# Performance work log

Measured on AMD Instinct MI355X. Metric: run time of the kernel, lower is better.

Reference implementation:

```python
import jax, jax.numpy as jnp
import numpy as np

P, B, FEAT, HID, ATTN, NHEAD = 4096, 32, 512, 512, 512, 8
HD = ATTN // NHEAD  # 64


def setup_inputs() -> dict:
    key = jax.random.key(0)
    ks = jax.random.split(key, 12)
    s = lambda n: 1.0 / np.sqrt(n)
    return {
        "last_hidden": jax.random.normal(ks[0], (1, B, HID), jnp.float32),
        "encoder_outputs": jax.random.normal(ks[1], (P, B, FEAT), jnp.float32),
        # outer projections (stored [in, out]; torch Linear is x @ W.T + b)
        "Wa_w": jax.random.uniform(ks[2], (FEAT, ATTN), jnp.float32, -s(FEAT), s(FEAT)),
        "Wa_b": jax.random.uniform(ks[3], (ATTN,), jnp.float32, -s(FEAT), s(FEAT)),
        "Ua_w": jax.random.uniform(ks[4], (HID, ATTN), jnp.float32, -s(HID), s(HID)),
        "Ua_b": jax.random.uniform(ks[5], (ATTN,), jnp.float32, -s(HID), s(HID)),
        # inner Attention(head_attn_size, head_attn_size, head_attn_size)
        "Wa2_w": jax.random.uniform(ks[6], (HD, HD), jnp.float32, -s(HD), s(HD)),
        "Wa2_b": jax.random.uniform(ks[7], (HD,), jnp.float32, -s(HD), s(HD)),
        "Ua2_w": jax.random.uniform(ks[8], (HD, HD), jnp.float32, -s(HD), s(HD)),
        "Ua2_b": jax.random.uniform(ks[9], (HD,), jnp.float32, -s(HD), s(HD)),
        "va_w": jax.random.uniform(ks[10], (HD, 1), jnp.float32, -s(HD), s(HD)),
        "va_b": jax.random.uniform(ks[11], (1,), jnp.float32, -s(HD), s(HD)),
        "nhead": NHEAD,
    }


def reference(last_hidden, encoder_outputs, Wa_w, Wa_b, Ua_w, Ua_b,
              Wa2_w, Wa2_b, Ua2_w, Ua2_b, va_w, va_b, nhead):
    p, b = encoder_outputs.shape[:2]
    enc = encoder_outputs @ Wa_w + Wa_b            # [P,B,A]
    hid = last_hidden @ Ua_w + Ua_b                # [1,B,A]
    hd = enc.shape[-1] // nhead
    enc = enc.reshape(p, b, nhead, hd)             # [P,B,nh,hd]
    hid = hid.reshape(1, b, nhead, hd)             # [1,B,nh,hd]
    # inner Bahdanau attention
    a = jnp.tanh((enc @ Wa2_w + Wa2_b) + (hid @ Ua2_w + Ua2_b))
    scores = a @ va_w + va_b                       # [P,B,nh,1]
    weights = jax.nn.softmax(scores, axis=0)       # softmax over pixels
    context = jnp.sum(weights * enc, axis=0, keepdims=True)  # [1,B,nh,hd]
    weight = jnp.mean(weights, axis=-2)            # mean over heads -> [P,B,1]
    context = context.reshape(1, b, nhead * hd)    # [1,B,A]
    return context, weight
```

## Files before the change

### kernel.cpp

```cpp
#include <hip/hip_runtime.h>
#include <hip/hip_bf16.h>

#define PDIM 4096
#define BDIM 32
#define MDIM (PDIM*BDIM)
#define KDIM 512
#define NDIM 512
#define NH   8
#define HD   64

typedef __attribute__((ext_vector_type(4))) float f32x4;
typedef __attribute__((ext_vector_type(8))) short bf16x8;

__device__ __forceinline__ unsigned short f2bf(float f) {
  unsigned u = __float_as_uint(f);
  u += 0x7fffu + ((u >> 16) & 1u);
  return (unsigned short)(u >> 16);
}
__device__ __forceinline__ float bf2f(unsigned short u) {
  return __uint_as_float(((unsigned)u) << 16);
}

__device__ __forceinline__ float fast_tanh(float x) {
  x = fminf(fmaxf(x, -15.f), 15.f);
  float e = __expf(2.f * x);
  return __fdividef(e - 1.f, e + 1.f);
}

#define GLOAD_LDS16(g, l) __builtin_amdgcn_global_load_lds( \
    (const __attribute__((address_space(1))) void*)(g),     \
    (__attribute__((address_space(3))) void*)(l), 16, 0, 0)

__global__ __launch_bounds__(256) void cvt_k(
    const float* __restrict__ x, unsigned short* __restrict__ xbf) {
  size_t i = ((size_t)blockIdx.x * 256 + threadIdx.x) * 8;
  float4 a = *(const float4*)(x + i);
  float4 b = *(const float4*)(x + i + 4);
  ushort4 o0; o0.x = f2bf(a.x); o0.y = f2bf(a.y); o0.z = f2bf(a.z); o0.w = f2bf(a.w);
  ushort4 o1; o1.x = f2bf(b.x); o1.y = f2bf(b.y); o1.z = f2bf(b.z); o1.w = f2bf(b.w);
  *(ushort4*)(xbf + i) = o0;
  *(ushort4*)(xbf + i + 4) = o1;
}

__global__ __launch_bounds__(512) void hub_k(
    const float* __restrict__ lh, const float* __restrict__ Ua,
    const float* __restrict__ Ua_b, const float* __restrict__ Ua2,
    const float* __restrict__ Ua2_b, const float* __restrict__ Wa_b,
    const float* __restrict__ Wa2, const float* __restrict__ Wa2_b,
    float* __restrict__ ubf) {
  int b = blockIdx.x, tid = threadIdx.x;
  __shared__ float ls[512];
  __shared__ float hs[512];
  ls[tid] = lh[b*512 + tid];
  __syncthreads();
  float s = Ua_b[tid];
  #pragma unroll 8
  for (int k = 0; k < 512; ++k)
    s += ls[k] * Ua[(size_t)k*512 + tid];
  hs[tid] = s;
  __syncthreads();
  int h = tid >> 6, j = tid & 63;
  float u = Ua2_b[j] + Wa2_b[j];
  #pragma unroll 4
  for (int k = 0; k < 64; ++k) {
    u += hs[h*64 + k] * Ua2[k*64 + j];
    u += Wa_b[h*64 + k] * Wa2[k*64 + j];
  }
  ubf[b*512 + tid] = u;
}

__global__ __launch_bounds__(256) void wft_k(
    const float* __restrict__ Wa, const float* __restrict__ Wa2,
    unsigned short* __restrict__ WfT) {
  int n = blockIdx.x, tid = threadIdx.x;
  int h = n >> 6, j = n & 63;
  __shared__ float w2[64];
  if (tid < 64) w2[tid] = Wa2[tid*64 + j];
  __syncthreads();
  for (int k = tid; k < 512; k += 256) {
    float s = 0.f;
    #pragma unroll 8
    for (int kk = 0; kk < 64; ++kk)
      s += Wa[(size_t)k*512 + h*64 + kk] * w2[kk];
    WfT[(size_t)n*512 + k] = f2bf(s);
  }
}

__global__ __launch_bounds__(256, 3) void gemm_score_k(
    const unsigned short* __restrict__ xbf, const unsigned short* __restrict__ WfT,
    const float* __restrict__ ubf, const float* __restrict__ va_w,
    const float* __restrict__ va_b, float* __restrict__ scores) {
  __shared__ __align__(16) unsigned short As[8192];
  __shared__ __align__(16) unsigned short Bs[8192];
  __shared__ float ubf_s[32*128];
  int tid = threadIdx.x;
  int bn = blockIdx.x, bm = blockIdx.y;
  int m0 = bm*128, n0 = bn*128;
  #pragma unroll
  for (int t = 0; t < 16; ++t) {
    int idx = t*256 + tid;
    ubf_s[idx] = ubf[(idx >> 7)*512 + n0 + (idx & 127)];
  }
  int lane = tid & 63, w = tid >> 6;
  int quad = lane >> 4, l16 = lane & 15;
  int wr = w >> 1, wc = w & 1;
  f32x4 acc[4][4] = {};

  for (int k0 = 0; k0 < KDIM; k0 += 64) {
    __syncthreads();
    #pragma unroll
    for (int i = 0; i < 4; ++i) {
      int c = i*256 + tid;
      int r = c & 127, kc = c >> 7;
      GLOAD_LDS16(xbf + (size_t)(m0 + r)*512 + k0 + kc*8, As + (size_t)c*8);
    }
    #pragma unroll
    for (int i = 0; i < 4; ++i) {
      int c = i*256 + tid;
      int r = c & 127, kc = c >> 7;
      GLOAD_LDS16(WfT + (size_t)(n0 + r)*512 + k0 + kc*8, Bs + (size_t)c*8);
    }
    __syncthreads();
    #pragma unroll
    for (int kk = 0; kk < 64; kk += 32) {
      int kc = (kk >> 3) + quad;
      bf16x8 af[4], bfr[4];
      #pragma unroll
      for (int ti = 0; ti < 4; ++ti)
        af[ti] = *(const bf16x8*)(As + ((size_t)kc*128 + 64*wr + 16*ti + l16)*8);
      #pragma unroll
      for (int tj = 0; tj < 4; ++tj)
        bfr[tj] = *(const bf16x8*)(Bs + ((size_t)kc*128 + 64*wc + 16*tj + l16)*8);
      #pragma unroll
      for (int ti = 0; ti < 4; ++ti)
        #pragma unroll
        for (int tj = 0; tj < 4; ++tj)
          acc[ti][tj] = __builtin_amdgcn_mfma_f32_16x16x32_bf16(
              af[ti], bfr[tj], acc[ti][tj], 0, 0, 0);
    }
  }

  int head = bn*2 + wc;
  float va_r[4];
  #pragma unroll
  for (int tj = 0; tj < 4; ++tj) va_r[tj] = va_w[16*tj + l16];
  float vb = va_b[0];
  #pragma unroll
  for (int ti = 0; ti < 4; ++ti) {
    #pragma unroll
    for (int r = 0; r < 4; ++r) {
      int row_loc = 64*wr + 16*ti + 4*quad + r;
      int b31 = row_loc & 31;
      float s = 0.f;
      #pragma unroll
      for (int tj = 0; tj < 4; ++tj) {
        float xa = acc[ti][tj][r] + ubf_s[b31*128 + 64*wc + 16*tj + l16];
        s += fast_tanh(xa) * va_r[tj];
      }
      s += __shfl_xor(s, 1); s += __shfl_xor(s, 2);
      s += __shfl_xor(s, 4); s += __shfl_xor(s, 8);
      if (l16 == 0) scores[(size_t)(m0 + row_loc)*NH + head] = s + vb;
    }
  }
}

__global__ __launch_bounds__(256) void softmax_k(
    const float* __restrict__ sc, float* __restrict__ w) {
  int b = blockIdx.x >> 3, h = blockIdx.x & 7;
  int tid = threadIdx.x;
  float v[16];
  float mx = -1e30f;
  #pragma unroll
  for (int i = 0; i < 16; ++i) {
    int p = tid + i*256;
    v[i] = sc[(size_t)(p*32 + b)*NH + h];
    mx = fmaxf(mx, v[i]);
  }
  for (int m = 1; m < 64; m <<= 1) mx = fmaxf(mx, __shfl_xor(mx, m));
  __shared__ float redm[4], reds[4];
  int wid = tid >> 6, lane = tid & 63;
  if (lane == 0) redm[wid] = mx;
  __syncthreads();
  mx = fmaxf(fmaxf(redm[0], redm[1]), fmaxf(redm[2], redm[3]));
  float sum = 0.f;
  #pragma unroll
  for (int i = 0; i < 16; ++i) { v[i] = __expf(v[i] - mx); sum += v[i]; }
  for (int m = 1; m < 64; m <<= 1) sum += __shfl_xor(sum, m);
  if (lane == 0) reds[wid] = sum;
  __syncthreads();
  sum = reds[0] + reds[1] + reds[2] + reds[3];
  float inv = 1.f / sum;
  #pragma unroll
  for (int i = 0; i < 16; ++i) {
    int p = tid + i*256;
    w[(size_t)(p*32 + b)*NH + h] = v[i] * inv;
  }
}

__global__ __launch_bounds__(256) void mean_k(
    const float* __restrict__ w, float* __restrict__ out) {
  int m = blockIdx.x*256 + threadIdx.x;
  const float4* p = (const float4*)(w + (size_t)m*NH);
  float4 a = p[0], c = p[1];
  out[BDIM*NDIM + m] = (a.x+a.y+a.z+a.w + c.x+c.y+c.z+c.w) * 0.125f;
}

__global__ __launch_bounds__(256) void ctx_partial_k(
    const unsigned short* __restrict__ xbf, const float* __restrict__ w,
    float* __restrict__ part) {
  int pc = blockIdx.x;
  int b  = blockIdx.y;
  int tid = threadIdx.x;
  __shared__ float wl[256*8];
  __shared__ float red[4][512];
  {
    const float4* wp = (const float4*)(w + ((size_t)((pc*256 + tid)*32 + b))*NH);
    float4 a = wp[0], c = wp[1];
    float4* dst = (float4*)(wl + tid*8);
    dst[0] = a; dst[1] = c;
  }
  __syncthreads();
  int lane = tid & 63, wv = tid >> 6;
  float acc[8][8];
  #pragma unroll
  for (int h = 0; h < 8; ++h)
    #pragma unroll
    for (int j = 0; j < 8; ++j) acc[h][j] = 0.f;
  for (int i = 0; i < 64; ++i) {
    int pl = wv*64 + i;
    bf16x8 xv = *(const bf16x8*)(xbf + ((size_t)((pc*256 + pl)*32 + b))*512 + lane*8);
    float xf[8];
    #pragma unroll
    for (int j = 0; j < 8; ++j) xf[j] = bf2f((unsigned short)xv[j]);
    #pragma unroll
    for (int h = 0; h < 8; ++h) {
      float ww = wl[pl*8 + h];
      #pragma unroll
      for (int j = 0; j < 8; ++j) acc[h][j] += ww * xf[j];
    }
  }
  for (int h = 0; h < 8; ++h) {
    #pragma unroll
    for (int j = 0; j < 8; j += 4)
      *(float4*)(&red[wv][lane*8 + j]) = *(float4*)(&acc[h][j]);
    __syncthreads();
    if (tid < 64) {
      #pragma unroll
      for (int j = 0; j < 8; ++j) {
        int f = tid*8 + j;
        part[((size_t)(b*16 + pc)*NH + h)*512 + f] =
            red[0][f] + red[1][f] + red[2][f] + red[3][f];
      }
    }
    __syncthreads();
  }
}

__global__ __launch_bounds__(256) void ctx_reduce_k(
    const float* __restrict__ part, float* __restrict__ cx) {
  int gid = blockIdx.x*256 + threadIdx.x;
  int f = gid & 511;
  int bh = gid >> 9;
  int h = bh & 7, b = bh >> 3;
  float s = 0.f;
  #pragma unroll
  for (int pc = 0; pc < 16; ++pc)
    s += part[((size_t)(b*16 + pc)*NH + h)*512 + f];
  cx[gid] = s;
}

__global__ __launch_bounds__(256) void ctx_proj_k(
    const float* __restrict__ cx, const float* __restrict__ Wa,
    const float* __restrict__ Wa_b, float* __restrict__ out) {
  int b = blockIdx.x >> 3, h = blockIdx.x & 7;
  int tid = threadIdx.x;
  __shared__ float cs[512];
  cs[tid]       = cx[(size_t)blockIdx.x*512 + tid];
  cs[tid + 256] = cx[(size_t)blockIdx.x*512 + tid + 256];
  __syncthreads();
  int d = tid & 63, g = tid >> 6;
  float s = 0.f;
  #pragma unroll 8
  for (int f = g*128; f < g*128 + 128; ++f)
    s += cs[f] * Wa[(size_t)f*512 + h*64 + d];
  __shared__ float red[256];
  red[tid] = s;
  __syncthreads();
  if (tid < 64) {
    float tot = red[tid] + red[64+tid] + red[128+tid] + red[192+tid] + Wa_b[h*64 + tid];
    out[b*512 + h*64 + tid] = tot;
  }
}

extern "C" void kernel_launch(void* const* d_in, const int* in_sizes, int n_in,
                              void* d_out, int out_size, void* d_ws, size_t ws_size,
                              hipStream_t stream) {
  (void)in_sizes; (void)n_in; (void)out_size; (void)ws_size;
  const float* lh    = (const float*)d_in[0];
  const float* x     = (const float*)d_in[1];
  const float* Wa_w  = (const float*)d_in[2];
  const float* Wa_b  = (const float*)d_in[3];
  const float* Ua_w  = (const float*)d_in[4];
  const float* Ua_b  = (const float*)d_in[5];
  const float* Wa2_w = (const float*)d_in[6];
  const float* Wa2_b = (const float*)d_in[7];
  const float* Ua2_w = (const float*)d_in[8];
  const float* Ua2_b = (const float*)d_in[9];
  const float* va_w  = (const float*)d_in[10];
  const float* va_b  = (const float*)d_in[11];
  float* out = (float*)d_out;
  char* ws = (char*)d_ws;

  unsigned short* xbf = (unsigned short*)(ws);
  unsigned short* WfT = (unsigned short*)(ws + 134217728);
  float* ubf    = (float*)(ws + 134742016);
  float* scores = (float*)(ws + 134807552);
  float* w      = (float*)(ws + 139001856);
  float* part   = (float*)(ws + 143196160);
  float* cx     = (float*)(ws + 151584768);

  hipLaunchKernelGGL(cvt_k, dim3(32768), dim3(256), 0, stream, x, xbf);
  hipLaunchKernelGGL(hub_k, dim3(32), dim3(512), 0, stream,
                     lh, Ua_w, Ua_b, Ua2_w, Ua2_b, Wa_b, Wa2_w, Wa2_b, ubf);
  hipLaunchKernelGGL(wft_k, dim3(512), dim3(256), 0, stream, Wa_w, Wa2_w, WfT);
  hipLaunchKernelGGL(gemm_score_k, dim3(4, 1024), dim3(256), 0, stream,
                     xbf, WfT, ubf, va_w, va_b, scores);
  hipLaunchKernelGGL(softmax_k, dim3(256), dim3(256), 0, stream, scores, w);
  hipLaunchKernelGGL(mean_k, dim3(512), dim3(256), 0, stream, w, out);
  hipLaunchKernelGGL(ctx_partial_k, dim3(16, 32), dim3(256), 0, stream, xbf, w, part);
  hipLaunchKernelGGL(ctx_reduce_k, dim3(512), dim3(256), 0, stream, part, cx);
  hipLaunchKernelGGL(ctx_proj_k, dim3(256), dim3(256), 0, stream, cx, Wa_w, Wa_b, out);
}
```

Baseline: 658.8 us.

## Double-buffer GEMM tiles, remap blocks, and transpose scores for coalesced softmax

The score GEMM now double-buffers its A/B LDS tiles so the next K-slice's global-to-LDS loads are issued before the current slice's MFMAs. It also uses a 1D grid with a block-index remap across groups of eight. The ubf tile is loaded into the reused A buffer after the main loop, with row padding to reduce LDS bank conflicts. Scores and weights are stored in a [head][batch][pixel] layout so softmax, mean and the context partial kernel read contiguous float4 or coalesced data instead of stride-8 accesses. The trade-offs are lower occupancy (launch bounds drop from 3 to 2), and mean_k now runs on only 16 blocks, each thread summing 256 values.

```diff
diff --git a/kernel.cpp b/kernel.cpp
--- a/kernel.cpp
+++ b/kernel.cpp
@@ -86,51 +86,66 @@
   }
 }
 
-__global__ __launch_bounds__(256, 3) void gemm_score_k(
+__global__ __launch_bounds__(256, 2) void gemm_score_k(
     const unsigned short* __restrict__ xbf, const unsigned short* __restrict__ WfT,
     const float* __restrict__ ubf, const float* __restrict__ va_w,
     const float* __restrict__ va_b, float* __restrict__ scores) {
-  __shared__ __align__(16) unsigned short As[8192];
-  __shared__ __align__(16) unsigned short Bs[8192];
-  __shared__ float ubf_s[32*128];
-  int tid = threadIdx.x;
-  int bn = blockIdx.x, bm = blockIdx.y;
+  __shared__ __align__(16) unsigned short As[2][8192];
+  __shared__ __align__(16) unsigned short Bs[2][8192];
+  int tid = threadIdx.x;
+  int orig = blockIdx.x;
+  int wg = (orig & 7) * 512 + (orig >> 3);
+  int bn = wg & 3, bm = wg >> 2;
   int m0 = bm*128, n0 = bn*128;
-  #pragma unroll
-  for (int t = 0; t < 16; ++t) {
-    int idx = t*256 + tid;
-    ubf_s[idx] = ubf[(idx >> 7)*512 + n0 + (idx & 127)];
-  }
   int lane = tid & 63, w = tid >> 6;
   int quad = lane >> 4, l16 = lane & 15;
   int wr = w >> 1, wc = w & 1;
   f32x4 acc[4][4] = {};
 
-  for (int k0 = 0; k0 < KDIM; k0 += 64) {
-    __syncthreads();
-    #pragma unroll
-    for (int i = 0; i < 4; ++i) {
-      int c = i*256 + tid;
-      int r = c & 127, kc = c >> 7;
-      GLOAD_LDS16(xbf + (size_t)(m0 + r)*512 + k0 + kc*8, As + (size_t)c*8);
-    }
-    #pragma unroll
-    for (int i = 0; i < 4; ++i) {
-      int c = i*256 + tid;
-      int r = c & 127, kc = c >> 7;
-      GLOAD_LDS16(WfT + (size_t)(n0 + r)*512 + k0 + kc*8, Bs + (size_t)c*8);
-    }
-    __syncthreads();
+  #pragma unroll
+  for (int i = 0; i < 4; ++i) {
+    int c = i*256 + tid;
+    int r = c & 127, kc = c >> 7;
+    GLOAD_LDS16(xbf + (size_t)(m0 + r)*512 + kc*8, &As[0][(size_t)c*8]);
+  }
+  #pragma unroll
+  for (int i = 0; i < 4; ++i) {
+    int c = i*256 + tid;
+    int r = c & 127, kc = c >> 7;
+    GLOAD_LDS16(WfT + (size_t)(n0 + r)*512 + kc*8, &Bs[0][(size_t)c*8]);
+  }
+  __syncthreads();
+
+  #pragma unroll
+  for (int t = 0; t < 8; ++t) {
+    int cur = t & 1, nxt = cur ^ 1;
+    if (t < 7) {
+      int kn = (t + 1) * 64;
+      #pragma unroll
+      for (int i = 0; i < 4; ++i) {
+        int c = i*256 + tid;
+        int r = c & 127, kc = c >> 7;
+        GLOAD_LDS16(xbf + (size_t)(m0 + r)*512 + kn + kc*8, &As[nxt][(size_t)c*8]);
+      }
+      #pragma unroll
+      for (int i = 0; i < 4; ++i) {
+        int c = i*256 + tid;
+        int r = c & 127, kc = c >> 7;
+        GLOAD_LDS16(WfT + (size_t)(n0 + r)*512 + kn + kc*8, &Bs[nxt][(size_t)c*8]);
+      }
+    }
+    const unsigned short* Ab = &As[cur][0];
+    const unsigned short* Bb = &Bs[cur][0];
     #pragma unroll
     for (int kk = 0; kk < 64; kk += 32) {
       int kc = (kk >> 3) + quad;
       bf16x8 af[4], bfr[4];
       #pragma unroll
       for (int ti = 0; ti < 4; ++ti)
-        af[ti] = *(const bf16x8*)(As + ((size_t)kc*128 + 64*wr + 16*ti + l16)*8);
+        af[ti] = *(const bf16x8*)(Ab + ((size_t)kc*128 + 64*wr + 16*ti + l16)*8);
       #pragma unroll
       for (int tj = 0; tj < 4; ++tj)
-        bfr[tj] = *(const bf16x8*)(Bs + ((size_t)kc*128 + 64*wc + 16*tj + l16)*8);
+        bfr[tj] = *(const bf16x8*)(Bb + ((size_t)kc*128 + 64*wc + 16*tj + l16)*8);
       #pragma unroll
       for (int ti = 0; ti < 4; ++ti)
         #pragma unroll
@@ -138,7 +153,17 @@
           acc[ti][tj] = __builtin_amdgcn_mfma_f32_16x16x32_bf16(
               af[ti], bfr[tj], acc[ti][tj], 0, 0, 0);
     }
-  }
+    __syncthreads();
+  }
+
+  float* ubf_s = (float*)&As[0][0];
+  #pragma unroll
+  for (int t = 0; t < 16; ++t) {
+    int idx = t*256 + tid;
+    int b = idx >> 7, c = idx & 127;
+    ubf_s[b*129 + c] = ubf[b*512 + n0 + c];
+  }
+  __syncthreads();
 
   int head = bn*2 + wc;
   float va_r[4];
@@ -154,28 +179,32 @@
       float s = 0.f;
       #pragma unroll
       for (int tj = 0; tj < 4; ++tj) {
-        float xa = acc[ti][tj][r] + ubf_s[b31*128 + 64*wc + 16*tj + l16];
+        float xa = acc[ti][tj][r] + ubf_s[b31*129 + 64*wc + 16*tj + l16];
         s += fast_tanh(xa) * va_r[tj];
       }
       s += __shfl_xor(s, 1); s += __shfl_xor(s, 2);
       s += __shfl_xor(s, 4); s += __shfl_xor(s, 8);
-      if (l16 == 0) scores[(size_t)(m0 + row_loc)*NH + head] = s + vb;
+      if (l16 == 0) {
+        int m = m0 + row_loc;
+        scores[((size_t)head*32 + (m & 31))*4096 + (m >> 5)] = s + vb;
+      }
     }
   }
 }
 
 __global__ __launch_bounds__(256) void softmax_k(
     const float* __restrict__ sc, float* __restrict__ w) {
-  int b = blockIdx.x >> 3, h = blockIdx.x & 7;
-  int tid = threadIdx.x;
-  float v[16];
+  int bh = blockIdx.x;
+  int tid = threadIdx.x;
+  const float* row = sc + (size_t)bh*4096;
+  float4 v[4];
   float mx = -1e30f;
   #pragma unroll
-  for (int i = 0; i < 16; ++i) {
-    int p = tid + i*256;
-    v[i] = sc[(size_t)(p*32 + b)*NH + h];
-    mx = fmaxf(mx, v[i]);
-  }
+  for (int i = 0; i < 4; ++i) {
+    v[i] = *(const float4*)(row + (size_t)(i*256 + tid)*4);
+    mx = fmaxf(mx, fmaxf(fmaxf(v[i].x, v[i].y), fmaxf(v[i].z, v[i].w)));
+  }
+  #pragma unroll
   for (int m = 1; m < 64; m <<= 1) mx = fmaxf(mx, __shfl_xor(mx, m));
   __shared__ float redm[4], reds[4];
   int wid = tid >> 6, lane = tid & 63;
@@ -184,25 +213,45 @@
   mx = fmaxf(fmaxf(redm[0], redm[1]), fmaxf(redm[2], redm[3]));
   float sum = 0.f;
   #pragma unroll
-  for (int i = 0; i < 16; ++i) { v[i] = __expf(v[i] - mx); sum += v[i]; }
+  for (int i = 0; i < 4; ++i) {
+    v[i].x = __expf(v[i].x - mx); v[i].y = __expf(v[i].y - mx);
+    v[i].z = __expf(v[i].z - mx); v[i].w = __expf(v[i].w - mx);
+    sum += v[i].x + v[i].y + v[i].z + v[i].w;
+  }
+  #pragma unroll
   for (int m = 1; m < 64; m <<= 1) sum += __shfl_xor(sum, m);
   if (lane == 0) reds[wid] = sum;
   __syncthreads();
   sum = reds[0] + reds[1] + reds[2] + reds[3];
   float inv = 1.f / sum;
-  #pragma unroll
-  for (int i = 0; i < 16; ++i) {
-    int p = tid + i*256;
-    w[(size_t)(p*32 + b)*NH + h] = v[i] * inv;
+  float* dst = w + (size_t)bh*4096;
+  #pragma unroll
+  for (int i = 0; i < 4; ++i) {
+    float4 o; o.x = v[i].x*inv; o.y = v[i].y*inv; o.z = v[i].z*inv; o.w = v[i].w*inv;
+    *(float4*)(dst + (size_t)(i*256 + tid)*4) = o;
   }
 }
 
 __global__ __launch_bounds__(256) void mean_k(
     const float* __restrict__ w, float* __restrict__ out) {
-  int m = blockIdx.x*256 + threadIdx.x;
-  const float4* p = (const float4*)(w + (size_t)m*NH);
-  float4 a = p[0], c = p[1];
-  out[BDIM*NDIM + m] = (a.x+a.y+a.z+a.w + c.x+c.y+c.z+c.w) * 0.125f;
+  int p0 = blockIdx.x * 256;
+  int tid = threadIdx.x;
+  float s[32];
+  #pragma unroll
+  for (int b = 0; b < 32; ++b) s[b] = 0.f;
+  for (int h = 0; h < 8; ++h) {
+    #pragma unroll
+    for (int b = 0; b < 32; ++b)
+      s[b] += w[((size_t)h*32 + b)*4096 + p0 + tid];
+  }
+  float4* dst = (float4*)(out + BDIM*NDIM + (size_t)(p0 + tid)*32);
+  #pragma unroll
+  for (int j = 0; j < 8; ++j) {
+    float4 o;
+    o.x = s[4*j]*0.125f; o.y = s[4*j+1]*0.125f;
+    o.z = s[4*j+2]*0.125f; o.w = s[4*j+3]*0.125f;
+    dst[j] = o;
+  }
 }
 
 __global__ __launch_bounds__(256) void ctx_partial_k(
@@ -211,14 +260,11 @@
   int pc = blockIdx.x;
   int b  = blockIdx.y;
   int tid = threadIdx.x;
-  __shared__ float wl[256*8];
+  __shared__ float wl[8*256];
   __shared__ float red[4][512];
-  {
-    const float4* wp = (const float4*)(w + ((size_t)((pc*256 + tid)*32 + b))*NH);
-    float4 a = wp[0], c = wp[1];
-    float4* dst = (float4*)(wl + tid*8);
-    dst[0] = a; dst[1] = c;
-  }
+  #pragma unroll
+  for (int h = 0; h < 8; ++h)
+    wl[h*256 + tid] = w[((size_t)h*32 + b)*4096 + pc*256 + tid];
   __syncthreads();
   int lane = tid & 63, wv = tid >> 6;
   float acc[8][8];
@@ -234,7 +280,7 @@
     for (int j = 0; j < 8; ++j) xf[j] = bf2f((unsigned short)xv[j]);
     #pragma unroll
     for (int h = 0; h < 8; ++h) {
-      float ww = wl[pl*8 + h];
+      float ww = wl[h*256 + pl];
       #pragma unroll
       for (int j = 0; j < 8; ++j) acc[h][j] += ww * xf[j];
     }
@@ -259,10 +305,10 @@
 __global__ __launch_bounds__(256) void ctx_reduce_k(
     const float* __restrict__ part, float* __restrict__ cx) {
   int gid = blockIdx.x*256 + threadIdx.x;
+  float s = 0.f;
   int f = gid & 511;
   int bh = gid >> 9;
   int h = bh & 7, b = bh >> 3;
-  float s = 0.f;
   #pragma unroll
   for (int pc = 0; pc < 16; ++pc)
     s += part[((size_t)(b*16 + pc)*NH + h)*512 + f];
@@ -323,10 +369,10 @@
   hipLaunchKernelGGL(hub_k, dim3(32), dim3(512), 0, stream,
                      lh, Ua_w, Ua_b, Ua2_w, Ua2_b, Wa_b, Wa2_w, Wa2_b, ubf);
   hipLaunchKernelGGL(wft_k, dim3(512), dim3(256), 0, stream, Wa_w, Wa2_w, WfT);
-  hipLaunchKernelGGL(gemm_score_k, dim3(4, 1024), dim3(256), 0, stream,
+  hipLaunchKernelGGL(gemm_score_k, dim3(4096), dim3(256), 0, stream,
                      xbf, WfT, ubf, va_w, va_b, scores);
   hipLaunchKernelGGL(softmax_k, dim3(256), dim3(256), 0, stream, scores, w);
-  hipLaunchKernelGGL(mean_k, dim3(512), dim3(256), 0, stream, w, out);
+  hipLaunchKernelGGL(mean_k, dim3(16), dim3(256), 0, stream, w, out);
   hipLaunchKernelGGL(ctx_partial_k, dim3(16, 32), dim3(256), 0, stream, xbf, w, part);
   hipLaunchKernelGGL(ctx_reduce_k, dim3(512), dim3(256), 0, stream, part, cx);
   hipLaunchKernelGGL(ctx_proj_k, dim3(256), dim3(256), 0, stream, cx, Wa_w, Wa_b, out);
```

New measurement: 684.1 us. +3.8%, slower.
